# Kernel tuning notes

Measured on AMD Instinct MI355X. Metric: run time of the kernel, lower is better.

The kernel has to match this reference:

```python
import jax, jax.numpy as jnp
import numpy as np

N_NODES = 100000


def gcn_conv(x, W, b, src, dst, n_nodes):
    """PyG GCNConv: add self-loops, symmetric normalization, linear, scatter-add, bias."""
    xw = x @ W  # [N, out]
    loop = jnp.arange(n_nodes, dtype=src.dtype)
    src2 = jnp.concatenate([src, loop])  # sources (x_j gathered from here)
    dst2 = jnp.concatenate([dst, loop])  # targets (aggregation index)
    # degree (incl. self-loops) computed at target nodes, unit edge weights
    deg = jax.ops.segment_sum(jnp.ones_like(dst2, dtype=xw.dtype), dst2, num_segments=n_nodes)
    dinv = jnp.where(deg > 0, jax.lax.rsqrt(deg), 0.0)
    norm = dinv[src2] * dinv[dst2]  # [E+N]
    msg = xw[src2] * norm[:, None]  # [E+N, out]  (memory-bound gather)
    out = jax.ops.segment_sum(msg, dst2, num_segments=n_nodes)  # scatter-add
    return out + b


def setup_inputs() -> dict:
    key = jax.random.key(0)
    k1, k2, k3, k4 = jax.random.split(key, 4)
    F_IN, H, C = 128, 128, 64
    E = 1600000
    x = jax.random.normal(k1, (N_NODES, F_IN), dtype=jnp.float32)
    edge_index = jax.random.randint(k2, (2, E), 0, N_NODES, dtype=jnp.int64)
    # Glorot init like PyG GCNConv
    s1 = float(np.sqrt(6.0 / (F_IN + H)))
    s2 = float(np.sqrt(6.0 / (H + C)))
    W1 = jax.random.uniform(k3, (F_IN, H), jnp.float32, -s1, s1)
    W2 = jax.random.uniform(k4, (H, C), jnp.float32, -s2, s2)
    b1 = jnp.zeros((H,), jnp.float32)
    b2 = jnp.zeros((C,), jnp.float32)
    return {"x": x, "edge_index": edge_index, "W1": W1, "b1": b1, "W2": W2, "b2": b2}


def reference(x, edge_index, W1, b1, W2, b2):
    src, dst = edge_index[0], edge_index[1]
    h = gcn_conv(x, W1, b1, src, dst, N_NODES)
    h = jax.nn.relu(h)  # dropout p=0.0 -> identity
    h = gcn_conv(h, W2, b2, src, dst, N_NODES)
    return jax.nn.log_softmax(h, axis=1)
```

## Files before the change

### kernel.cpp

```cpp
#include <hip/hip_runtime.h>
#include <cmath>


#define THREADS 256
#define BSHIFT 8
#define MAXB 512
#define SLAB_E 8192
#define SLAB_C 9984
#define NB_CAST 96
#define ECHUNK 4096

__device__ __forceinline__ unsigned short f2bf(float f) {
    union { float f; unsigned u; } v; v.f = f;
    unsigned r = v.u + 0x7FFFu + ((v.u >> 16) & 1u);
    return (unsigned short)(r >> 16);
}
__device__ __forceinline__ float bf_lo(unsigned u) {
    union { unsigned u; float f; } v; v.u = u << 16; return v.f;
}
__device__ __forceinline__ float bf_hi(unsigned u) {
    union { unsigned u; float f; } v; v.u = u & 0xFFFF0000u; return v.f;
}

typedef __attribute__((ext_vector_type(8))) short bf16x8;
typedef __attribute__((ext_vector_type(4))) float f32x4;

__global__ __launch_bounds__(256) void k_bscatter(const int* __restrict__ src,
                                                  const int* __restrict__ dst, int E, int B,
                                                  const float* __restrict__ W1,
                                                  const float* __restrict__ W2,
                                                  unsigned short* __restrict__ Wt1,
                                                  unsigned short* __restrict__ Wt2,
                                                  int* __restrict__ bfill,
                                                  unsigned* __restrict__ pairs) {
    const int tid = threadIdx.x;
    if (blockIdx.x < NB_CAST) {
        int idx = blockIdx.x * 256 + tid;
        if (idx < 16384) {
            int n = idx >> 7, k = idx & 127;
            Wt1[idx] = f2bf(W1[k * 128 + n]);
        } else {
            int t = idx - 16384;
            int n = t >> 7, k = t & 127;
            Wt2[t] = f2bf(W2[k * 64 + n]);
        }
        return;
    }
    __shared__ int lc[MAXB];
    __shared__ int lbase[MAXB];
    const int e0 = (blockIdx.x - NB_CAST) * ECHUNK;
    for (int i = tid; i < MAXB; i += 256) lc[i] = 0;
    __syncthreads();
#pragma unroll
    for (int k = 0; k < ECHUNK / 1024; k++) {
        int e = e0 + k * 1024 + tid * 4;
        if (e < E) {
            int4 d4 = *(const int4*)&dst[e];
            atomicAdd(&lc[d4.x >> BSHIFT], 1); atomicAdd(&lc[d4.y >> BSHIFT], 1);
            atomicAdd(&lc[d4.z >> BSHIFT], 1); atomicAdd(&lc[d4.w >> BSHIFT], 1);
        }
    }
    __syncthreads();
    for (int b = tid; b < B; b += 256)
        lbase[b] = lc[b] ? atomicAdd(&bfill[b], lc[b]) : 0;
    __syncthreads();
    for (int i = tid; i < MAXB; i += 256) lc[i] = 0;
    __syncthreads();
#pragma unroll
    for (int k = 0; k < ECHUNK / 1024; k++) {
        int e = e0 + k * 1024 + tid * 4;
        if (e < E) {
            int4 s4 = *(const int4*)&src[e];
            int4 d4 = *(const int4*)&dst[e];
            int b0, r;
            b0 = d4.x >> BSHIFT; r = atomicAdd(&lc[b0], 1);
            pairs[(size_t)b0 * SLAB_E + lbase[b0] + r] = ((unsigned)(d4.x & 255) << 24) | (unsigned)s4.x;
            b0 = d4.y >> BSHIFT; r = atomicAdd(&lc[b0], 1);
            pairs[(size_t)b0 * SLAB_E + lbase[b0] + r] = ((unsigned)(d4.y & 255) << 24) | (unsigned)s4.y;
            b0 = d4.z >> BSHIFT; r = atomicAdd(&lc[b0], 1);
            pairs[(size_t)b0 * SLAB_E + lbase[b0] + r] = ((unsigned)(d4.z & 255) << 24) | (unsigned)s4.z;
            b0 = d4.w >> BSHIFT; r = atomicAdd(&lc[b0], 1);
            pairs[(size_t)b0 * SLAB_E + lbase[b0] + r] = ((unsigned)(d4.w & 255) << 24) | (unsigned)s4.w;
        }
    }
}

__global__ __launch_bounds__(256) void k_bbuild(const unsigned* __restrict__ pairs,
                                                const int* __restrict__ bfill, int N,
                                                int* __restrict__ deg,
                                                float* __restrict__ dinv,
                                                int* __restrict__ rowptr,
                                                unsigned* __restrict__ csr_off) {
    __shared__ int ldeg[256], lex[256], lrank[256];
    const int b = blockIdx.x, tid = threadIdx.x;
    const int node0 = b << BSHIFT;
    const unsigned* pb = pairs + (size_t)b * SLAB_E;
    const int cnt_e = bfill[b];
    const int pbase = b * SLAB_C;
    ldeg[tid] = 0;
    __syncthreads();
    for (int e = tid; e < cnt_e; e += 256)
        atomicAdd(&ldeg[pb[e] >> 24], 1);
    __syncthreads();
    int v = ldeg[tid];
    int pd = (v + 7) & ~7;
    lex[tid] = pd; __syncthreads();
    for (int o = 1; o < 256; o <<= 1) {
        int add = (tid >= o) ? lex[tid - o] : 0;
        __syncthreads();
        lex[tid] += add;
        __syncthreads();
    }
    int pexcl = lex[tid] - pd;
    if (node0 + tid < N) {
        deg[node0 + tid] = v;
        dinv[node0 + tid] = rsqrtf((float)(v + 1));
        rowptr[node0 + tid] = pbase + pexcl;
    }
    __syncthreads();
    lex[tid] = pexcl;
    lrank[tid] = 0;
    __syncthreads();
    for (int e = tid; e < cnt_e; e += 256) {
        unsigned p = pb[e];
        int loc = p >> 24;
        int r = atomicAdd(&lrank[loc], 1);
        csr_off[pbase + lex[loc] + r] = (p & 0xFFFFFFu) << 8;
    }
    for (int p = v; p < pd; p++)
        csr_off[pbase + pexcl + p] = ((unsigned)N) << 8;
}

template <int NC, bool A_BF16>
__global__ __launch_bounds__(256) void k_gemm_mfma(const void* __restrict__ Av,
                                                   const unsigned short* __restrict__ Wt,
                                                   const float* __restrict__ dinv,
                                                   unsigned short* __restrict__ Out,
                                                   unsigned short* __restrict__ zrow,
                                                   int M) {
    constexpr int KP = 136;
    __shared__ __align__(16) short Bs[NC * KP];
    const int tid = threadIdx.x;
    const int row0 = blockIdx.x * 64;

    if (blockIdx.x == 0 && tid < NC) zrow[tid] = 0;

    for (int f = tid; f < NC * 16; f += 256) {
        int n = f >> 4, c = (f & 15) * 8;
        *(uint4*)&Bs[n * KP + c] = *(const uint4*)&Wt[n * 128 + c];
    }

    const int wave = tid >> 6, lane = tid & 63;
    const int m = lane & 15, quad = lane >> 4;
    const int row = row0 + 16 * wave + m;
    const int rowc = row < M ? row : (M - 1);

    bf16x8 afr[4];
    if (A_BF16) {
        const unsigned short* A = (const unsigned short*)Av;
#pragma unroll
        for (int k = 0; k < 4; k++)
            afr[k] = *(const bf16x8*)&A[(size_t)rowc * 128 + quad * 8 + 32 * k];
    } else {
        const float* A = (const float*)Av;
#pragma unroll
        for (int k = 0; k < 4; k++) {
            float4 lo = *(const float4*)&A[(size_t)rowc * 128 + quad * 8 + 32 * k];
            float4 hi = *(const float4*)&A[(size_t)rowc * 128 + quad * 8 + 32 * k + 4];
            bf16x8 a;
            a[0] = (short)f2bf(lo.x); a[1] = (short)f2bf(lo.y);
            a[2] = (short)f2bf(lo.z); a[3] = (short)f2bf(lo.w);
            a[4] = (short)f2bf(hi.x); a[5] = (short)f2bf(hi.y);
            a[6] = (short)f2bf(hi.z); a[7] = (short)f2bf(hi.w);
            afr[k] = a;
        }
    }
    __syncthreads();

    constexpr int CT = NC / 16;
    f32x4 acc[CT] = {};
    const short* brow = &Bs[m * KP + quad * 8];
#pragma unroll
    for (int k = 0; k < 4; k++) {
#pragma unroll
        for (int c = 0; c < CT; c++) {
            bf16x8 b = *(const bf16x8*)&brow[(size_t)c * 16 * KP + 32 * k];
            acc[c] = __builtin_amdgcn_mfma_f32_16x16x32_bf16(afr[k], b, acc[c], 0, 0, 0);
        }
    }

    __syncthreads();
    short* Cs = Bs;
    const int rbase = 16 * wave + quad * 4;
    float dv[4];
#pragma unroll
    for (int r = 0; r < 4; r++) {
        int gr = row0 + rbase + r;
        dv[r] = dinv[gr < M ? gr : 0];
    }
#pragma unroll
    for (int c = 0; c < CT; c++)
#pragma unroll
        for (int r = 0; r < 4; r++)
            Cs[(rbase + r) * NC + 16 * c + m] = (short)f2bf(acc[c][r] * dv[r]);
    __syncthreads();
    for (int f = tid; f < 64 * NC / 8; f += 256) {
        int r = f / (NC / 8), c = (f % (NC / 8)) * 8;
        if (row0 + r < M)
            *(uint4*)&Out[(size_t)(row0 + r) * NC + c] = *(const uint4*)&Cs[r * NC + c];
    }
}

__global__ __launch_bounds__(256) void k_agg128b(const unsigned* __restrict__ csr_off,
                                                 const int* __restrict__ rowptr,
                                                 const int* __restrict__ cnt,
                                                 const float* __restrict__ dinv,
                                                 const unsigned char* __restrict__ xwb,
                                                 const float* __restrict__ bias,
                                                 unsigned* __restrict__ h1, int N) {
    const int lane = threadIdx.x & 63;
    const int wid = (blockIdx.x * blockDim.x + threadIdx.x) >> 6;
    const int g = lane >> 4, sl = lane & 15;
    const int i = wid * 4 + g;
    if (i >= N) return;
    const float di = dinv[i];
    const int slb = sl * 16;
    uint4 u = *(const uint4*)(xwb + ((size_t)i << 8) + slb);
    float a0 = bf_lo(u.x), a1 = bf_hi(u.x), a2 = bf_lo(u.y), a3 = bf_hi(u.y);
    float a4 = bf_lo(u.z), a5 = bf_hi(u.z), a6 = bf_lo(u.w), a7 = bf_hi(u.w);
    const int start = rowptr[i];
    const int pc = (cnt[i] + 7) & ~7;
    unsigned s[8];
#pragma unroll
    for (int k = 0; k < 8; k++) s[k] = csr_off[start + k];
    for (int j = 0; j < pc; j += 8) {
        uint4 uu[8];
#pragma unroll
        for (int k = 0; k < 8; k++) uu[k] = *(const uint4*)(xwb + s[k] + slb);
#pragma unroll
        for (int k = 0; k < 8; k++) s[k] = csr_off[start + j + 8 + k];
#pragma unroll
        for (int k = 0; k < 8; k++) {
            a0 += bf_lo(uu[k].x); a1 += bf_hi(uu[k].x);
            a2 += bf_lo(uu[k].y); a3 += bf_hi(uu[k].y);
            a4 += bf_lo(uu[k].z); a5 += bf_hi(uu[k].z);
            a6 += bf_lo(uu[k].w); a7 += bf_hi(uu[k].w);
        }
    }
    float4 b0 = *(const float4*)&bias[8 * sl];
    float4 b1 = *(const float4*)&bias[8 * sl + 4];
    float r0 = fmaxf(di * a0 + b0.x, 0.f);
    float r1 = fmaxf(di * a1 + b0.y, 0.f);
    float r2 = fmaxf(di * a2 + b0.z, 0.f);
    float r3 = fmaxf(di * a3 + b0.w, 0.f);
    float r4 = fmaxf(di * a4 + b1.x, 0.f);
    float r5 = fmaxf(di * a5 + b1.y, 0.f);
    float r6 = fmaxf(di * a6 + b1.z, 0.f);
    float r7 = fmaxf(di * a7 + b1.w, 0.f);
    uint4 o;
    o.x = (unsigned)f2bf(r0) | ((unsigned)f2bf(r1) << 16);
    o.y = (unsigned)f2bf(r2) | ((unsigned)f2bf(r3) << 16);
    o.z = (unsigned)f2bf(r4) | ((unsigned)f2bf(r5) << 16);
    o.w = (unsigned)f2bf(r6) | ((unsigned)f2bf(r7) << 16);
    *(uint4*)&h1[(size_t)i * 64 + 4 * sl] = o;
}

__global__ __launch_bounds__(256) void k_agg64b(const unsigned* __restrict__ csr_off,
                                                const int* __restrict__ rowptr,
                                                const int* __restrict__ cnt,
                                                const float* __restrict__ dinv,
                                                const unsigned char* __restrict__ xwb,
                                                const float* __restrict__ bias,
                                                float* __restrict__ out, int N) {
    const int lane = threadIdx.x & 63;
    const int wid = (blockIdx.x * blockDim.x + threadIdx.x) >> 6;
    const int g = lane >> 3, sl = lane & 7;
    const int i = wid * 8 + g;
    if (i >= N) return;
    const float di = dinv[i];
    const int slb = sl * 16;
    uint4 u = *(const uint4*)(xwb + ((size_t)i << 7) + slb);
    float a0 = bf_lo(u.x), a1 = bf_hi(u.x), a2 = bf_lo(u.y), a3 = bf_hi(u.y);
    float a4 = bf_lo(u.z), a5 = bf_hi(u.z), a6 = bf_lo(u.w), a7 = bf_hi(u.w);
    const int start = rowptr[i];
    const int pc = (cnt[i] + 7) & ~7;
    unsigned s[8];
#pragma unroll
    for (int k = 0; k < 8; k++) s[k] = csr_off[start + k];
    for (int j = 0; j < pc; j += 8) {
        uint4 uu[8];
#pragma unroll
        for (int k = 0; k < 8; k++) uu[k] = *(const uint4*)(xwb + (s[k] >> 1) + slb);
#pragma unroll
        for (int k = 0; k < 8; k++) s[k] = csr_off[start + j + 8 + k];
#pragma unroll
        for (int k = 0; k < 8; k++) {
            a0 += bf_lo(uu[k].x); a1 += bf_hi(uu[k].x);
            a2 += bf_lo(uu[k].y); a3 += bf_hi(uu[k].y);
            a4 += bf_lo(uu[k].z); a5 += bf_hi(uu[k].z);
            a6 += bf_lo(uu[k].w); a7 += bf_hi(uu[k].w);
        }
    }
    float4 b0 = *(const float4*)&bias[8 * sl];
    float4 b1 = *(const float4*)&bias[8 * sl + 4];
    float v0 = di * a0 + b0.x, v1 = di * a1 + b0.y;
    float v2 = di * a2 + b0.z, v3 = di * a3 + b0.w;
    float v4 = di * a4 + b1.x, v5 = di * a5 + b1.y;
    float v6 = di * a6 + b1.z, v7 = di * a7 + b1.w;
    float m = fmaxf(fmaxf(fmaxf(v0, v1), fmaxf(v2, v3)),
                    fmaxf(fmaxf(v4, v5), fmaxf(v6, v7)));
#pragma unroll
    for (int o = 4; o > 0; o >>= 1) m = fmaxf(m, __shfl_xor(m, o));
    float s2 = expf(v0 - m) + expf(v1 - m) + expf(v2 - m) + expf(v3 - m) +
               expf(v4 - m) + expf(v5 - m) + expf(v6 - m) + expf(v7 - m);
#pragma unroll
    for (int o = 4; o > 0; o >>= 1) s2 += __shfl_xor(s2, o);
    float ls = m + logf(s2);
    *(float4*)&out[(size_t)i * 64 + 8 * sl] = make_float4(v0 - ls, v1 - ls, v2 - ls, v3 - ls);
    *(float4*)&out[(size_t)i * 64 + 8 * sl + 4] = make_float4(v4 - ls, v5 - ls, v6 - ls, v7 - ls);
}

extern "C" void kernel_launch(void* const* d_in, const int* in_sizes, int n_in,
                              void* d_out, int out_size, void* d_ws, size_t ws_size,
                              hipStream_t stream) {
    const float* x  = (const float*)d_in[0];
    const int*   ei = (const int*)d_in[1];
    const float* W1 = (const float*)d_in[2];
    const float* b1 = (const float*)d_in[3];
    const float* W2 = (const float*)d_in[4];
    const float* b2 = (const float*)d_in[5];

    const int N = in_sizes[0] / 128;
    const int E = in_sizes[1] / 2;
    const int* src = ei;
    const int* dst = ei + E;
    const int B = (N + 255) >> BSHIFT;
    const int NBLK = (E + ECHUNK - 1) / ECHUNK;

    char* ws = (char*)d_ws;
    size_t off = 0;
    auto alloc = [&](size_t bytes) {
        void* p = ws + off;
        off += (bytes + 255) & ~(size_t)255;
        return p;
    };
    int*            bfill   = (int*)alloc(MAXB * 4);
    int*            deg     = (int*)alloc((size_t)N * 4);
    float*          dinv    = (float*)alloc((size_t)N * 4);
    int*            rowptr  = (int*)alloc((size_t)N * 4);
    unsigned*       csr_off = (unsigned*)alloc(((size_t)B * SLAB_C + 64) * 4);
    unsigned*       pairs   = (unsigned*)alloc((size_t)B * SLAB_E * 4);
    unsigned short* Wt1     = (unsigned short*)alloc(128 * 128 * 2);
    unsigned short* Wt2     = (unsigned short*)alloc(64 * 128 * 2);
    unsigned short* xw1     = (unsigned short*)alloc((size_t)(N + 1) * 128 * 2);
    unsigned short* h1      = (unsigned short*)alloc((size_t)N * 128 * 2);
    unsigned short* hw2     = xw1;
    float*          outp    = (float*)d_out;

    hipMemsetAsync(bfill, 0, MAXB * 4, stream);

    k_bscatter<<<NB_CAST + NBLK, THREADS, 0, stream>>>(src, dst, E, B, W1, W2, Wt1, Wt2,
                                                       bfill, pairs);
    k_bbuild<<<B, THREADS, 0, stream>>>(pairs, bfill, N, deg, dinv, rowptr, csr_off);

    k_gemm_mfma<128, false><<<(N + 63) / 64, THREADS, 0, stream>>>(
        x, Wt1, dinv, xw1, xw1 + (size_t)N * 128, N);
    k_agg128b<<<(N + 15) / 16, THREADS, 0, stream>>>(
        csr_off, rowptr, deg, dinv, (const unsigned char*)xw1, b1, (unsigned*)h1, N);

    k_gemm_mfma<64, true><<<(N + 63) / 64, THREADS, 0, stream>>>(
        h1, Wt2, dinv, hw2, hw2 + (size_t)N * 64, N);
    k_agg64b<<<(N + 31) / 32, THREADS, 0, stream>>>(
        csr_off, rowptr, deg, dinv, (const unsigned char*)hw2, b2, outp, N);
}
```

Baseline: 251.3 us.

## Fuse layer-2 GEMM into layer-1 aggregation kernel via LDS MFMA

The layer-1 aggregation kernel now keeps its 16 aggregated bf16 rows in shared memory and multiplies them by W2 with MFMA in the same block. It then scales by dinv and writes hw2 directly. This removes the separate second GEMM launch and the round trip of the h1 intermediate through global memory. In exchange, every 16-node block reloads the 64x128 W2 tile into LDS and adds two more barriers, and the larger LDS footprint may lower occupancy of the gather-bound aggregation.

```diff
diff --git a/kernel.cpp b/kernel.cpp
--- a/kernel.cpp
+++ b/kernel.cpp
@@ -131,14 +131,13 @@
         csr_off[pbase + pexcl + p] = ((unsigned)N) << 8;
 }
 
-template <int NC, bool A_BF16>
-__global__ __launch_bounds__(256) void k_gemm_mfma(const void* __restrict__ Av,
-                                                   const unsigned short* __restrict__ Wt,
-                                                   const float* __restrict__ dinv,
-                                                   unsigned short* __restrict__ Out,
-                                                   unsigned short* __restrict__ zrow,
-                                                   int M) {
-    constexpr int KP = 136;
+__global__ __launch_bounds__(256) void k_gemm1(const float* __restrict__ A,
+                                               const unsigned short* __restrict__ Wt,
+                                               const float* __restrict__ dinv,
+                                               unsigned short* __restrict__ Out,
+                                               unsigned short* __restrict__ zrow,
+                                               int M) {
+    constexpr int NC = 128, KP = 136;
     __shared__ __align__(16) short Bs[NC * KP];
     const int tid = threadIdx.x;
     const int row0 = blockIdx.x * 64;
@@ -156,24 +155,16 @@
     const int rowc = row < M ? row : (M - 1);
 
     bf16x8 afr[4];
-    if (A_BF16) {
-        const unsigned short* A = (const unsigned short*)Av;
-#pragma unroll
-        for (int k = 0; k < 4; k++)
-            afr[k] = *(const bf16x8*)&A[(size_t)rowc * 128 + quad * 8 + 32 * k];
-    } else {
-        const float* A = (const float*)Av;
-#pragma unroll
-        for (int k = 0; k < 4; k++) {
-            float4 lo = *(const float4*)&A[(size_t)rowc * 128 + quad * 8 + 32 * k];
-            float4 hi = *(const float4*)&A[(size_t)rowc * 128 + quad * 8 + 32 * k + 4];
-            bf16x8 a;
-            a[0] = (short)f2bf(lo.x); a[1] = (short)f2bf(lo.y);
-            a[2] = (short)f2bf(lo.z); a[3] = (short)f2bf(lo.w);
-            a[4] = (short)f2bf(hi.x); a[5] = (short)f2bf(hi.y);
-            a[6] = (short)f2bf(hi.z); a[7] = (short)f2bf(hi.w);
-            afr[k] = a;
-        }
+#pragma unroll
+    for (int k = 0; k < 4; k++) {
+        float4 lo = *(const float4*)&A[(size_t)rowc * 128 + quad * 8 + 32 * k];
+        float4 hi = *(const float4*)&A[(size_t)rowc * 128 + quad * 8 + 32 * k + 4];
+        bf16x8 a;
+        a[0] = (short)f2bf(lo.x); a[1] = (short)f2bf(lo.y);
+        a[2] = (short)f2bf(lo.z); a[3] = (short)f2bf(lo.w);
+        a[4] = (short)f2bf(hi.x); a[5] = (short)f2bf(hi.y);
+        a[6] = (short)f2bf(hi.z); a[7] = (short)f2bf(hi.w);
+        afr[k] = a;
     }
     __syncthreads();
 
@@ -211,25 +202,41 @@
     }
 }
 
-__global__ __launch_bounds__(256) void k_agg128b(const unsigned* __restrict__ csr_off,
-                                                 const int* __restrict__ rowptr,
-                                                 const int* __restrict__ cnt,
-                                                 const float* __restrict__ dinv,
-                                                 const unsigned char* __restrict__ xwb,
-                                                 const float* __restrict__ bias,
-                                                 unsigned* __restrict__ h1, int N) {
-    const int lane = threadIdx.x & 63;
-    const int wid = (blockIdx.x * blockDim.x + threadIdx.x) >> 6;
+__global__ __launch_bounds__(256) void k_agg128g2(const unsigned* __restrict__ csr_off,
+                                                  const int* __restrict__ rowptr,
+                                                  const int* __restrict__ cnt,
+                                                  const float* __restrict__ dinv,
+                                                  const unsigned char* __restrict__ xwb,
+                                                  const float* __restrict__ bias,
+                                                  const unsigned short* __restrict__ Wt2,
+                                                  unsigned short* __restrict__ hw2,
+                                                  unsigned short* __restrict__ zrow,
+                                                  int N) {
+    constexpr int KP = 136;
+    __shared__ __align__(16) short Bs[64 * KP];
+    __shared__ __align__(16) short As[16 * KP];
+    const int tid = threadIdx.x;
+    const int lane = tid & 63, wave = tid >> 6;
     const int g = lane >> 4, sl = lane & 15;
-    const int i = wid * 4 + g;
-    if (i >= N) return;
-    const float di = dinv[i];
+    const int node0 = blockIdx.x * 16;
+    const int i = node0 + wave * 4 + g;
+    const bool active = (i < N);
+    const int ic = active ? i : 0;
+
+    if (blockIdx.x == 0 && tid < 64) zrow[tid] = 0;
+
+    for (int f = tid; f < 64 * 16; f += 256) {
+        int n = f >> 4, c = (f & 15) * 8;
+        *(uint4*)&Bs[n * KP + c] = *(const uint4*)&Wt2[n * 128 + c];
+    }
+
+    const float di = dinv[ic];
     const int slb = sl * 16;
-    uint4 u = *(const uint4*)(xwb + ((size_t)i << 8) + slb);
+    uint4 u = *(const uint4*)(xwb + ((size_t)ic << 8) + slb);
     float a0 = bf_lo(u.x), a1 = bf_hi(u.x), a2 = bf_lo(u.y), a3 = bf_hi(u.y);
     float a4 = bf_lo(u.z), a5 = bf_hi(u.z), a6 = bf_lo(u.w), a7 = bf_hi(u.w);
-    const int start = rowptr[i];
-    const int pc = (cnt[i] + 7) & ~7;
+    const int start = rowptr[ic];
+    const int pc = active ? ((cnt[ic] + 7) & ~7) : 0;
     unsigned s[8];
 #pragma unroll
     for (int k = 0; k < 8; k++) s[k] = csr_off[start + k];
@@ -262,7 +269,36 @@
     o.y = (unsigned)f2bf(r2) | ((unsigned)f2bf(r3) << 16);
     o.z = (unsigned)f2bf(r4) | ((unsigned)f2bf(r5) << 16);
     o.w = (unsigned)f2bf(r6) | ((unsigned)f2bf(r7) << 16);
-    *(uint4*)&h1[(size_t)i * 64 + 4 * sl] = o;
+    *(uint4*)&As[(wave * 4 + g) * KP + 8 * sl] = o;
+    __syncthreads();
+
+    const int m = lane & 15, quad = lane >> 4;
+    f32x4 acc = {};
+    const short* arow = &As[m * KP + quad * 8];
+    const short* brow = &Bs[(16 * wave + m) * KP + quad * 8];
+#pragma unroll
+    for (int k = 0; k < 4; k++) {
+        bf16x8 a = *(const bf16x8*)&arow[32 * k];
+        bf16x8 b = *(const bf16x8*)&brow[32 * k];
+        acc = __builtin_amdgcn_mfma_f32_16x16x32_bf16(a, b, acc, 0, 0, 0);
+    }
+    __syncthreads();
+    short* Cs = As;
+    float dv[4];
+#pragma unroll
+    for (int r = 0; r < 4; r++) {
+        int gr = node0 + quad * 4 + r;
+        dv[r] = dinv[gr < N ? gr : 0];
+    }
+#pragma unroll
+    for (int r = 0; r < 4; r++)
+        Cs[(quad * 4 + r) * 64 + 16 * wave + m] = (short)f2bf(acc[r] * dv[r]);
+    __syncthreads();
+    for (int f = tid; f < 128; f += 256) {
+        int r = f >> 3, c = (f & 7) * 8;
+        if (node0 + r < N)
+            *(uint4*)&hw2[(size_t)(node0 + r) * 64 + c] = *(const uint4*)&Cs[r * 64 + c];
+    }
 }
 
 __global__ __launch_bounds__(256) void k_agg64b(const unsigned* __restrict__ csr_off,
@@ -353,8 +389,7 @@
     unsigned short* Wt1     = (unsigned short*)alloc(128 * 128 * 2);
     unsigned short* Wt2     = (unsigned short*)alloc(64 * 128 * 2);
     unsigned short* xw1     = (unsigned short*)alloc((size_t)(N + 1) * 128 * 2);
-    unsigned short* h1      = (unsigned short*)alloc((size_t)N * 128 * 2);
-    unsigned short* hw2     = xw1;
+    unsigned short* hw2     = (unsigned short*)alloc((size_t)(N + 1) * 64 * 2);
     float*          outp    = (float*)d_out;
 
     hipMemsetAsync(bfill, 0, MAXB * 4, stream);
@@ -363,13 +398,11 @@
                                                        bfill, pairs);
     k_bbuild<<<B, THREADS, 0, stream>>>(pairs, bfill, N, deg, dinv, rowptr, csr_off);
 
-    k_gemm_mfma<128, false><<<(N + 63) / 64, THREADS, 0, stream>>>(
+    k_gemm1<<<(N + 63) / 64, THREADS, 0, stream>>>(
         x, Wt1, dinv, xw1, xw1 + (size_t)N * 128, N);
-    k_agg128b<<<(N + 15) / 16, THREADS, 0, stream>>>(
-        csr_off, rowptr, deg, dinv, (const unsigned char*)xw1, b1, (unsigned*)h1, N);
-
-    k_gemm_mfma<64, true><<<(N + 63) / 64, THREADS, 0, stream>>>(
-        h1, Wt2, dinv, hw2, hw2 + (size_t)N * 64, N);
+    k_agg128g2<<<(N + 15) / 16, THREADS, 0, stream>>>(
+        csr_off, rowptr, deg, dinv, (const unsigned char*)xw1, b1, Wt2,
+        hw2, hw2 + (size_t)N * 64, N);
     k_agg64b<<<(N + 31) / 32, THREADS, 0, stream>>>(
         csr_off, rowptr, deg, dinv, (const unsigned char*)hw2, b2, outp, N);
 }
```

New measurement: 240.2 us, median of 2. 1.05x faster.
